# Performance work log

Hardware: AMD Instinct MI355X
Metric: run time of the kernel (lower is better)

## Reference

```python
import jax, jax.numpy as jnp
import numpy as np

E, H, L = 512, 1024, 4
VS, VT = 32000, 32000
B, SS, TT = 64, 48, 48
PAD = 0


def _cell(x, h, c, Wih, Whh, bih, bhh):
    # torch.nn.LSTMCell math: gate order i, f, g, o
    g = x @ Wih.T + h @ Whh.T + bih + bhh
    i, f, gg, o = jnp.split(g, 4, axis=-1)
    c = jax.nn.sigmoid(f) * c + jax.nn.sigmoid(i) * jnp.tanh(gg)
    h = jax.nn.sigmoid(o) * jnp.tanh(c)
    return h, c


def setup_inputs() -> dict:
    key = jax.random.key(0)
    ks = jax.random.split(key, 14)
    s = 0.05
    d = {}
    d['src_tokens'] = jax.random.randint(ks[0], (SS, B), 0, VS, dtype=jnp.int32)
    d['tgt_tokens'] = jax.random.randint(ks[1], (TT, B), 0, VT, dtype=jnp.int32)
    d['src_emb'] = jax.random.normal(ks[2], (VS, E)) * s
    d['tgt_emb'] = jax.random.normal(ks[3], (VT, E)) * s
    d['enc_Wih0'] = jax.random.normal(ks[4], (4 * H, E)) * s
    d['enc_WihR'] = jax.random.normal(ks[5], (L - 1, 4 * H, H)) * s
    d['enc_Whh'] = jax.random.normal(ks[6], (L, 4 * H, H)) * s
    d['enc_bih'] = jnp.zeros((L, 4 * H))
    d['enc_bhh'] = jnp.zeros((L, 4 * H))
    d['dec_Wih0'] = jax.random.normal(ks[7], (4 * H, E + H)) * s
    d['dec_WihR'] = jax.random.normal(ks[8], (L - 1, 4 * H, H)) * s
    d['dec_Whh'] = jax.random.normal(ks[9], (L, 4 * H, H)) * s
    d['dec_bih'] = jnp.zeros((L, 4 * H))
    d['dec_bhh'] = jnp.zeros((L, 4 * H))
    d['att_vec_W'] = jax.random.normal(ks[10], (H, 2 * H)) * s
    d['readout_W'] = jax.random.normal(ks[11], (VT, H)) * s
    return d


def _forward(src_tokens, tgt_tokens, src_emb, tgt_emb, enc_Wih0, enc_WihR,
             enc_Whh, enc_bih, enc_bhh, dec_Wih0, dec_WihR, dec_Whh, dec_bih,
             dec_bhh, att_vec_W, readout_W):
    src_x = src_emb[src_tokens]                      # [SS, B, E]
    h0 = jnp.zeros((L, B, H), src_emb.dtype)
    c0 = jnp.zeros((L, B, H), src_emb.dtype)

    def enc_step(carry, x_t):
        h, c = carry
        inp = x_t
        hs, cs = [], []
        for l in range(L):
            Wih = enc_Wih0 if l == 0 else enc_WihR[l - 1]
            hn, cn = _cell(inp, h[l], c[l], Wih, enc_Whh[l], enc_bih[l], enc_bhh[l])
            hs.append(hn); cs.append(cn)
            inp = hn
        return (jnp.stack(hs), jnp.stack(cs)), inp

    (hT, cT), enc_out = jax.lax.scan(enc_step, (h0, c0), src_x)
    src_enc = enc_out.transpose(1, 0, 2)             # [B, SS, H]

    # decoder init: last encoder layer (h, c) copied to every decoder layer
    hd = jnp.tile(hT[-1][None], (L, 1, 1))
    cd = jnp.tile(cT[-1][None], (L, 1, 1))
    tgt_x = tgt_emb[tgt_tokens[:-1]]                 # [TT-1, B, E]
    att0 = jnp.zeros((B, H), src_emb.dtype)

    def dec_step(carry, y_t):
        h, c, att = carry
        inp = jnp.concatenate([y_t, att], axis=-1)   # input feeding
        hs, cs = [], []
        for l in range(L):
            Wih = dec_Wih0 if l == 0 else dec_WihR[l - 1]
            hn, cn = _cell(inp, h[l], c[l], Wih, dec_Whh[l], dec_bih[l], dec_bhh[l])
            hs.append(hn); cs.append(cn)
            inp = hn
        h_top = hs[-1]
        # global attention, 'dot' score (full-length seqs -> all-zero mask is a no-op)
        scores = jnp.einsum('bsh,bh->bs', src_enc, h_top)
        alpha = jax.nn.softmax(scores, axis=-1)
        ctx = jnp.einsum('bs,bsh->bh', alpha, src_enc)
        att_t = jnp.tanh(jnp.concatenate([h_top, ctx], axis=-1) @ att_vec_W.T)
        return (jnp.stack(hs), jnp.stack(cs), att_t), att_t

    _, att_ves = jax.lax.scan(dec_step, (hd, cd, att0), tgt_x)  # [TT-1, B, H]

    logp = jax.nn.log_softmax(att_ves @ readout_W.T, axis=-1)   # [TT-1, B, VT]
    gold = tgt_tokens[1:]
    gold_lp = jnp.take_along_axis(logp, gold[..., None], axis=-1)[..., 0]
    mask = (gold != PAD).astype(logp.dtype)
    return (gold_lp * mask).sum(axis=0)              # [B]


def reference(src_tokens, tgt_tokens, src_emb, tgt_emb, enc_Wih0, enc_WihR,
              enc_Whh, enc_bih, enc_bhh, dec_Wih0, dec_WihR, dec_Whh, dec_bih,
              dec_bhh, att_vec_W, readout_W):
    return _forward(src_tokens, tgt_tokens, src_emb, tgt_emb, enc_Wih0,
                    enc_WihR, enc_Whh, enc_bih, enc_bhh, dec_Wih0, dec_WihR,
                    dec_Whh, dec_bih, dec_bhh, att_vec_W, readout_W)
```

## Files before the change

kernel.cpp:

```cpp
#include <hip/hip_runtime.h>


typedef __attribute__((ext_vector_type(8))) short bf16x8;
typedef __attribute__((ext_vector_type(4))) float f32x4;

#define SMEM_BYTES 32768
#define SMEM_RO    49152

#define NMT_SYNC_LIGHT()                                   \
  do {                                                     \
    asm volatile("s_waitcnt lgkmcnt(0)" ::: "memory");     \
    __builtin_amdgcn_s_barrier();                          \
    __builtin_amdgcn_sched_barrier(0);                     \
  } while (0)

__device__ __forceinline__ float bf2f(ushort u) {
  union { uint i; float f; } v; v.i = ((uint)u) << 16; return v.f;
}
__device__ __forceinline__ ushort f2bf(float x) {
  union { float f; uint i; } v; v.f = x;
  uint r = (v.i + 0x7fffu + ((v.i >> 16) & 1u)) >> 16;
  return (ushort)r;
}
__device__ __forceinline__ float sigm(float x) {
  return __fdividef(1.f, 1.f + __expf(-x));
}
__device__ __forceinline__ float tanhf_fast(float x) {
  const float e = __expf(2.f * x);
  return 1.f - __fdividef(2.f, e + 1.f);
}

__device__ __forceinline__ void gemm_term(
    const ushort* __restrict__ A, int lda,
    const ushort* __restrict__ W, int ldw,
    int K, int m0, int n0,
    f32x4 acc[4], char* s)
{
  char* sA0 = s;
  char* sB0 = s + 8192;
  char* sA1 = s + 16384;
  char* sB1 = s + 24576;
  const int tid = threadIdx.x;
  const int lane = tid & 63;
  const int w = tid >> 6;
  const int r0 = tid >> 3;
  const int cge = (tid & 7) << 3;
  const ushort* Arow0 = A + (size_t)(m0 + r0) * lda + cge;
  const ushort* Arow1 = A + (size_t)(m0 + r0 + 32) * lda + cge;
  const ushort* Wrow0 = W + (size_t)(n0 + r0) * ldw + cge;
  const ushort* Wrow1 = W + (size_t)(n0 + r0 + 32) * ldw + cge;
  const int so0 = r0 * 128 + (((tid & 7) << 4) ^ ((r0 & 7) << 4));
  const int so1 = so0 + 4096;

  uint4 a0 = *reinterpret_cast<const uint4*>(Arow0);
  uint4 a1 = *reinterpret_cast<const uint4*>(Arow1);
  uint4 b0 = *reinterpret_cast<const uint4*>(Wrow0);
  uint4 b1 = *reinterpret_cast<const uint4*>(Wrow1);
  *reinterpret_cast<uint4*>(sA0 + so0) = a0;
  *reinterpret_cast<uint4*>(sA0 + so1) = a1;
  *reinterpret_cast<uint4*>(sB0 + so0) = b0;
  *reinterpret_cast<uint4*>(sB0 + so1) = b1;
  if (K > 64) {
    a0 = *reinterpret_cast<const uint4*>(Arow0 + 64);
    a1 = *reinterpret_cast<const uint4*>(Arow1 + 64);
    b0 = *reinterpret_cast<const uint4*>(Wrow0 + 64);
    b1 = *reinterpret_cast<const uint4*>(Wrow1 + 64);
  }
  const int axor = (lane & 7) << 4;
  const int arow = (w * 16 + (lane & 15)) * 128;
  const int brow = (lane & 15) * 128;
  const int kb0 = (lane >> 4) << 4;
  for (int kt = 0; kt < K; kt += 64) {
    char* cA = (kt & 64) ? sA1 : sA0;
    char* cB = (kt & 64) ? sB1 : sB0;
    char* nA = (kt & 64) ? sA0 : sA1;
    char* nB = (kt & 64) ? sB0 : sB1;
    __syncthreads();
    if (kt + 64 < K) {
      *reinterpret_cast<uint4*>(nA + so0) = a0;
      *reinterpret_cast<uint4*>(nA + so1) = a1;
      *reinterpret_cast<uint4*>(nB + so0) = b0;
      *reinterpret_cast<uint4*>(nB + so1) = b1;
      if (kt + 128 < K) {
        a0 = *reinterpret_cast<const uint4*>(Arow0 + kt + 128);
        a1 = *reinterpret_cast<const uint4*>(Arow1 + kt + 128);
        b0 = *reinterpret_cast<const uint4*>(Wrow0 + kt + 128);
        b1 = *reinterpret_cast<const uint4*>(Wrow1 + kt + 128);
      }
    }
#pragma unroll
    for (int ks = 0; ks < 2; ++ks) {
      const int kb = ks * 64 + kb0;
      bf16x8 af = *reinterpret_cast<const bf16x8*>(cA + arow + (kb ^ axor));
#pragma unroll
      for (int nf = 0; nf < 4; ++nf) {
        bf16x8 bfr = *reinterpret_cast<const bf16x8*>(
            cB + nf * 2048 + brow + (kb ^ axor));
        acc[nf] = __builtin_amdgcn_mfma_f32_16x16x32_bf16(af, bfr, acc[nf], 0, 0, 0);
      }
    }
  }
  __syncthreads();
}

__device__ __forceinline__ void store_f32(
    float* __restrict__ out, int ldo, int m0, int n0, f32x4 acc[4])
{
  const int tid = threadIdx.x, lane = tid & 63, w = tid >> 6;
  const int rbase = w * 16 + ((lane >> 4) << 2);
  const int cb = lane & 15;
#pragma unroll
  for (int nf = 0; nf < 4; ++nf)
#pragma unroll
    for (int r = 0; r < 4; ++r)
      out[(size_t)(m0 + rbase + r) * ldo + n0 + nf * 16 + cb] = acc[nf][r];
}

__device__ __forceinline__ void cell_store(
    float* smemF, f32x4 acc[4],
    float* __restrict__ c, ushort* __restrict__ hout,
    ushort* __restrict__ senc_t, int j0)
{
  const int tid = threadIdx.x, lane = tid & 63, w = tid >> 6;
  const int rbase = w * 16 + ((lane >> 4) << 2);
  const int cb = lane & 15;
  __syncthreads();
#pragma unroll
  for (int nf = 0; nf < 4; ++nf)
#pragma unroll
    for (int r = 0; r < 4; ++r)
      smemF[(rbase + r) * 68 + nf * 16 + cb] = acc[nf][r];
  __syncthreads();
#pragma unroll
  for (int i = 0; i < 4; ++i) {
    const int id = tid + i * 256;
    const int b = id >> 4, u = id & 15;
    const float g0 = smemF[b * 68 + u * 4 + 0];
    const float g1 = smemF[b * 68 + u * 4 + 1];
    const float g2 = smemF[b * 68 + u * 4 + 2];
    const float g3 = smemF[b * 68 + u * 4 + 3];
    const int off = b * 1024 + j0 + u;
    const float cold = c[off];
    const float cn = sigm(g1) * cold + sigm(g0) * tanhf_fast(g2);
    const float hv = sigm(g3) * tanhf_fast(cn);
    c[off] = cn;
    const ushort hb = f2bf(hv);
    hout[off] = hb;
    if (senc_t) senc_t[(size_t)b * 49152 + j0 + u] = hb;
  }
}

__global__ __launch_bounds__(256) void nmt_init(float* c, ushort* henc, ushort* attbf)
{
  const int idx = blockIdx.x * 256 + threadIdx.x;
  if (idx < 262144) c[idx] = 0.f;
  if (idx < 65536) {
    attbf[idx] = 0;
    henc[idx] = 0;
    henc[(size_t)1 * 49 * 65536 + idx] = 0;
    henc[(size_t)2 * 49 * 65536 + idx] = 0;
    henc[(size_t)3 * 49 * 65536 + idx] = 0;
  }
}

__global__ __launch_bounds__(256) void nmt_convperm(
    const float* __restrict__ in, ushort* __restrict__ out,
    int L, int Kin, int col0, int Kout)
{
  const size_t idx = (size_t)blockIdx.x * 256 + threadIdx.x;
  const size_t total = (size_t)L * 4096 * Kout;
  if (idx >= total) return;
  const int k = (int)(idx % Kout);
  const size_t rem = idx / Kout;
  const int rp = (int)(rem % 4096);
  const int l = (int)(rem / 4096);
  const int j = rp >> 2, g = rp & 3;
  out[idx] = f2bf(in[((size_t)l * 4096 + g * 1024 + j) * Kin + col0 + k]);
}

__global__ __launch_bounds__(256) void nmt_convplain(
    const float* __restrict__ in, ushort* __restrict__ out, size_t n)
{
  const size_t idx = (size_t)blockIdx.x * 256 + threadIdx.x;
  if (idx < n) out[idx] = f2bf(in[idx]);
}

__global__ __launch_bounds__(256) void nmt_bias(
    const float* __restrict__ bih, const float* __restrict__ bhh, float* __restrict__ bc)
{
  const int idx = blockIdx.x * 256 + threadIdx.x;
  if (idx >= 4 * 4096) return;
  const int rp = idx & 4095, l = idx >> 12;
  const int j = rp >> 2, g = rp & 3;
  bc[idx] = bih[l * 4096 + g * 1024 + j] + bhh[l * 4096 + g * 1024 + j];
}

__global__ __launch_bounds__(256) void nmt_gather(
    const int* __restrict__ tok, const float* __restrict__ emb,
    ushort* __restrict__ out, int rows)
{
  const size_t idx = (size_t)blockIdx.x * 256 + threadIdx.x;
  if (idx >= (size_t)rows * 512) return;
  const int k = (int)(idx & 511);
  const int r = (int)(idx >> 9);
  out[idx] = f2bf(emb[(size_t)tok[r] * 512 + k]);
}

__global__ __launch_bounds__(256) void nmt_pre(
    const ushort* __restrict__ A, const ushort* __restrict__ Wp,
    const float* __restrict__ bc0, float* __restrict__ out, int K)
{
  __shared__ __align__(16) char smem[SMEM_BYTES];
  const int m0 = blockIdx.x * 64, n0 = blockIdx.y * 64;
  const int lane = threadIdx.x & 63;
  const int cb = lane & 15;
  f32x4 acc[4];
#pragma unroll
  for (int nf = 0; nf < 4; ++nf) {
    const float bv = bc0[n0 + nf * 16 + cb];
#pragma unroll
    for (int r = 0; r < 4; ++r) acc[nf][r] = bv;
  }
  gemm_term(A, K, Wp, K, K, m0, n0, acc, smem);
  store_f32(out, 4096, m0, n0, acc);
}

__global__ __launch_bounds__(256) void nmt_decinit(
    const ushort* __restrict__ henc, float* c, ushort* h)
{
  const int idx = blockIdx.x * 256 + threadIdx.x;
  if (idx >= 65536) return;
  const ushort hv = henc[((size_t)3 * 49 + 48) * 65536 + idx];
  const float cv = c[3 * 65536 + idx];
  c[idx] = cv; c[65536 + idx] = cv; c[2 * 65536 + idx] = cv;
  h[idx] = hv; h[65536 + idx] = hv; h[2 * 65536 + idx] = hv; h[3 * 65536 + idx] = hv;
}

__global__ __launch_bounds__(256) void nmt_sv(
    const ushort* __restrict__ senc, const ushort* __restrict__ attW,
    ushort* __restrict__ SV)
{
  __shared__ __align__(16) char smem[SMEM_BYTES];
  const int b = blockIdx.x;
  const int n0 = blockIdx.y * 64;
  const int tid = threadIdx.x, lane = tid & 63, w = tid >> 6;
  const int rbase = w * 16 + ((lane >> 4) << 2), cb = lane & 15;
  f32x4 acc[4];
#pragma unroll
  for (int nf = 0; nf < 4; ++nf)
#pragma unroll
    for (int r = 0; r < 4; ++r) acc[nf][r] = 0.f;
  gemm_term(senc + (size_t)b * 49152, 1024, attW + 1024, 2048, 1024, 0, n0,
            acc, smem);
#pragma unroll
  for (int nf = 0; nf < 4; ++nf)
#pragma unroll
    for (int r = 0; r < 4; ++r) {
      const int row = rbase + r;
      if (row < 48)
        SV[(size_t)b * 49152 + row * 1024 + n0 + nf * 16 + cb] = f2bf(acc[nf][r]);
    }
}

__global__ __launch_bounds__(256) void nmt_enc_tick(
    int v, int lc0, int ncell, int lp0,
    ushort* __restrict__ henc, ushort* __restrict__ srcenc,
    float* __restrict__ c,
    const ushort* __restrict__ WihR, const ushort* __restrict__ Whh,
    const float* __restrict__ X0, const float* __restrict__ bcE,
    float* __restrict__ pbufE)
{
  __shared__ __align__(16) char smem[SMEM_BYTES];
  const int n0 = blockIdx.x * 64;
  const int tid = threadIdx.x, lane = tid & 63, w = tid >> 6;
  const int rbase = w * 16 + ((lane >> 4) << 2), cb = lane & 15;
  f32x4 acc[4];
  if ((int)blockIdx.y < ncell) {
    const int l = lc0 + blockIdx.y;
    const int t = v - 2 * l;
    if (l == 0) {
#pragma unroll
      for (int nf = 0; nf < 4; ++nf)
#pragma unroll
        for (int r = 0; r < 4; ++r)
          acc[nf][r] = X0[(size_t)t * 262144 + (size_t)(rbase + r) * 4096 + n0 + nf * 16 + cb];
    } else {
#pragma unroll
      for (int nf = 0; nf < 4; ++nf)
#pragma unroll
        for (int r = 0; r < 4; ++r)
          acc[nf][r] = pbufE[(size_t)l * 262144 + (size_t)(rbase + r) * 4096 + n0 + nf * 16 + cb];
    }
    gemm_term(henc + ((size_t)l * 49 + t) * 65536, 1024,
              Whh + (size_t)l * 4194304, 1024, 1024, 0, n0, acc, smem);
    cell_store((float*)smem, acc, c + l * 65536,
               henc + ((size_t)l * 49 + t + 1) * 65536,
               (l == 3) ? (srcenc + t * 1024) : (ushort*)nullptr, n0 >> 2);
  } else {
    const int l = lp0 + (blockIdx.y - ncell);
    const int tp = v + 1 - 2 * l;
#pragma unroll
    for (int nf = 0; nf < 4; ++nf) {
      const float bv = bcE[l * 4096 + n0 + nf * 16 + cb];
#pragma unroll
      for (int r = 0; r < 4; ++r) acc[nf][r] = bv;
    }
    gemm_term(henc + ((size_t)(l - 1) * 49 + tp + 1) * 65536, 1024,
              WihR + (size_t)(l - 1) * 4194304, 1024, 1024, 0, n0, acc, smem);
    store_f32(pbufE + (size_t)l * 262144, 4096, 0, n0, acc);
  }
}

__global__ __launch_bounds__(256) void nmt_dec_stage(
    int l, const ushort* __restrict__ hp, ushort* __restrict__ hn,
    float* __restrict__ c,
    const ushort* __restrict__ Whh, const ushort* __restrict__ WihR,
    const ushort* __restrict__ Wd0a, const ushort* __restrict__ attbf,
    const float* __restrict__ Y0t, const float* __restrict__ bcD,
    float* __restrict__ pbuf)
{
  __shared__ __align__(16) char smem[SMEM_BYTES];
  const int n0 = blockIdx.x * 64;
  const int tid = threadIdx.x, lane = tid & 63, w = tid >> 6;
  const int rbase = w * 16 + ((lane >> 4) << 2), cb = lane & 15;
  f32x4 acc[4];
  if (blockIdx.y == 0) {
    if (l == 0) {
#pragma unroll
      for (int nf = 0; nf < 4; ++nf)
#pragma unroll
        for (int r = 0; r < 4; ++r) {
          const size_t o = (size_t)(rbase + r) * 4096 + n0 + nf * 16 + cb;
          acc[nf][r] = Y0t[o] + pbuf[o];
        }
      gemm_term(attbf, 1024, Wd0a, 1024, 1024, 0, n0, acc, smem);
    } else {
#pragma unroll
      for (int nf = 0; nf < 4; ++nf)
#pragma unroll
        for (int r = 0; r < 4; ++r)
          acc[nf][r] = pbuf[(size_t)l * 262144 + (size_t)(rbase + r) * 4096 + n0 + nf * 16 + cb];
      gemm_term(hn + (l - 1) * 65536, 1024, WihR + (size_t)(l - 1) * 4194304,
                1024, 1024, 0, n0, acc, smem);
    }
    cell_store((float*)smem, acc, c + l * 65536, hn + l * 65536,
               (ushort*)nullptr, n0 >> 2);
  } else {
    const int lp = (l + 1) & 3;
    if (lp == 0) {
#pragma unroll
      for (int nf = 0; nf < 4; ++nf)
#pragma unroll
        for (int r = 0; r < 4; ++r) acc[nf][r] = 0.f;
      gemm_term(hn, 1024, Whh, 1024, 1024, 0, n0, acc, smem);
    } else {
#pragma unroll
      for (int nf = 0; nf < 4; ++nf) {
        const float bv = bcD[lp * 4096 + n0 + nf * 16 + cb];
#pragma unroll
        for (int r = 0; r < 4; ++r) acc[nf][r] = bv;
      }
      gemm_term(hp + lp * 65536, 1024, Whh + (size_t)lp * 4194304,
                1024, 1024, 0, n0, acc, smem);
    }
    store_f32(pbuf + (size_t)lp * 262144, 4096, 0, n0, acc);
  }
}

__global__ __launch_bounds__(256) void nmt_partial0(
    const ushort* __restrict__ h0, const ushort* __restrict__ Whh0,
    float* __restrict__ pbuf)
{
  __shared__ __align__(16) char smem[SMEM_BYTES];
  const int n0 = blockIdx.x * 64;
  f32x4 acc[4];
#pragma unroll
  for (int nf = 0; nf < 4; ++nf)
#pragma unroll
    for (int r = 0; r < 4; ++r) acc[nf][r] = 0.f;
  gemm_term(h0, 1024, Whh0, 1024, 1024, 0, n0, acc, smem);
  store_f32(pbuf, 4096, 0, n0, acc);
}

__global__ __launch_bounds__(256) void nmt_attnAB(
    const ushort* __restrict__ h3, const ushort* __restrict__ senc,
    const ushort* __restrict__ SV, const ushort* __restrict__ attW,
    float* __restrict__ ctx2, float* __restrict__ hb)
{
  __shared__ __align__(16) char smem[SMEM_BYTES];
  const int bid = blockIdx.x;
  const int tid = threadIdx.x, lane = tid & 63, w = tid >> 6;
  if (bid < 64) {
    float* sc = (float*)smem;
    float* al = (float*)smem + 64;
    const int b = bid;
    const ushort* sb = senc + (size_t)b * 49152;
    const ushort* vb = SV + (size_t)b * 49152;
    float hreg[16];
#pragma unroll
    for (int q = 0; q < 16; ++q) hreg[q] = bf2f(h3[b * 1024 + lane * 16 + q]);
    for (int s = w; s < 48; s += 4) {
      const ushort* vr = sb + s * 1024 + lane * 16;
      float p = 0.f;
#pragma unroll
      for (int q = 0; q < 16; ++q) p += bf2f(vr[q]) * hreg[q];
      for (int d = 1; d < 64; d <<= 1) p += __shfl_xor(p, d);
      if (lane == 0) sc[s] = p;
    }
    __syncthreads();
    if (tid < 64) {
      const float v = (lane < 48) ? sc[lane] : -3.4e38f;
      float m = v;
      for (int d = 1; d < 64; d <<= 1) m = fmaxf(m, __shfl_xor(m, d));
      float e = (lane < 48) ? expf(v - m) : 0.f;
      float s = e;
      for (int d = 1; d < 64; d <<= 1) s += __shfl_xor(s, d);
      al[lane] = e / s;
    }
    __syncthreads();
    const int k0 = tid * 4;
    float a0 = 0, a1 = 0, a2 = 0, a3 = 0;
    for (int s = 0; s < 48; ++s) {
      const float als = al[s];
      const ushort* vr = vb + s * 1024 + k0;
      a0 += als * bf2f(vr[0]); a1 += als * bf2f(vr[1]);
      a2 += als * bf2f(vr[2]); a3 += als * bf2f(vr[3]);
    }
    ctx2[b * 1024 + k0 + 0] = a0; ctx2[b * 1024 + k0 + 1] = a1;
    ctx2[b * 1024 + k0 + 2] = a2; ctx2[b * 1024 + k0 + 3] = a3;
  } else {
    const int n0 = (bid - 64) * 64;
    f32x4 acc[4];
#pragma unroll
    for (int nf = 0; nf < 4; ++nf)
#pragma unroll
      for (int r = 0; r < 4; ++r) acc[nf][r] = 0.f;
    gemm_term(h3, 1024, attW, 2048, 1024, 0, n0, acc, smem);
    store_f32(hb, 1024, 0, n0, acc);
  }
}

__global__ __launch_bounds__(256) void nmt_attnSB(
    const float* __restrict__ ctx2, const float* __restrict__ hb,
    ushort* __restrict__ attbf, ushort* __restrict__ av_t)
{
  const int base = blockIdx.x * 1024 + threadIdx.x * 4;
#pragma unroll
  for (int k = 0; k < 4; ++k) {
    const int i = base + k;
    const ushort us = f2bf(tanhf_fast(hb[i] + ctx2[i]));
    attbf[i] = us;
    av_t[i] = us;
  }
}

__global__ __launch_bounds__(256) void nmt_readout(
    const ushort* __restrict__ attves, const ushort* __restrict__ routW,
    const int* __restrict__ tgt, float* __restrict__ pmax,
    float* __restrict__ psum, float* __restrict__ goldl)
{
  __shared__ __align__(16) char smem[SMEM_RO];
  const int g = blockIdx.x;
  const int n0 = blockIdx.y * 64;
  const int tid = threadIdx.x, lane = tid & 63, w = tid >> 6;
  const int rbase = w * 16 + ((lane >> 4) << 2), cb = lane & 15;
  const int r0 = tid >> 3;
  const int cge = (tid & 7) << 3;
  const int soX = r0 * 128 + (((tid & 7) << 4) ^ ((r0 & 7) << 4));
  const int axor = (lane & 7) << 4;
  const int arow = (w * 16 + (lane & 15)) * 128;
  const int brow = (lane & 15) * 128;
  const int kb0 = (lane >> 4) << 4;

  const ushort* A0r0 = attves + (size_t)(g * 128 + r0) * 1024 + cge;
  const ushort* A0r1 = attves + (size_t)(g * 128 + r0 + 32) * 1024 + cge;
  const ushort* A1r0 = attves + (size_t)(g * 128 + 64 + r0) * 1024 + cge;
  const ushort* A1r1 = attves + (size_t)(g * 128 + 64 + r0 + 32) * 1024 + cge;
  const ushort* Br0  = routW + (size_t)(n0 + r0) * 1024 + cge;
  const ushort* Br1  = routW + (size_t)(n0 + r0 + 32) * 1024 + cge;

  f32x4 acc[2][4];
#pragma unroll
  for (int mi = 0; mi < 2; ++mi)
#pragma unroll
    for (int nf = 0; nf < 4; ++nf)
#pragma unroll
      for (int r = 0; r < 4; ++r) acc[mi][nf][r] = 0.f;

  uint4 ra0 = *(const uint4*)(A0r0);
  uint4 ra1 = *(const uint4*)(A0r1);
  uint4 ra2 = *(const uint4*)(A1r0);
  uint4 ra3 = *(const uint4*)(A1r1);
  uint4 rb0 = *(const uint4*)(Br0);
  uint4 rb1 = *(const uint4*)(Br1);
  {
    char* sl = smem;
    *(uint4*)(sl + soX) = ra0;          *(uint4*)(sl + 4096 + soX) = ra1;
    *(uint4*)(sl + 8192 + soX) = ra2;   *(uint4*)(sl + 12288 + soX) = ra3;
    *(uint4*)(sl + 16384 + soX) = rb0;  *(uint4*)(sl + 20480 + soX) = rb1;
  }
  ra0 = *(const uint4*)(A0r0 + 64);
  ra1 = *(const uint4*)(A0r1 + 64);
  ra2 = *(const uint4*)(A1r0 + 64);
  ra3 = *(const uint4*)(A1r1 + 64);
  rb0 = *(const uint4*)(Br0 + 64);
  rb1 = *(const uint4*)(Br1 + 64);

  for (int kt = 0; kt < 1024; kt += 64) {
    NMT_SYNC_LIGHT();
    if (kt + 64 < 1024) {
      char* sl = smem + ((((kt >> 6) + 1) & 1) ? 24576 : 0);
      *(uint4*)(sl + soX) = ra0;          *(uint4*)(sl + 4096 + soX) = ra1;
      *(uint4*)(sl + 8192 + soX) = ra2;   *(uint4*)(sl + 12288 + soX) = ra3;
      *(uint4*)(sl + 16384 + soX) = rb0;  *(uint4*)(sl + 20480 + soX) = rb1;
      if (kt + 128 < 1024) {
        ra0 = *(const uint4*)(A0r0 + kt + 128);
        ra1 = *(const uint4*)(A0r1 + kt + 128);
        ra2 = *(const uint4*)(A1r0 + kt + 128);
        ra3 = *(const uint4*)(A1r1 + kt + 128);
        rb0 = *(const uint4*)(Br0 + kt + 128);
        rb1 = *(const uint4*)(Br1 + kt + 128);
      }
    }
    char* cur = smem + (((kt >> 6) & 1) ? 24576 : 0);
#pragma unroll
    for (int ks = 0; ks < 2; ++ks) {
      const int kb = (ks << 6) + kb0;
      bf16x8 bf0 = *(const bf16x8*)(cur + 16384 + 0 * 2048 + brow + (kb ^ axor));
      bf16x8 bf1 = *(const bf16x8*)(cur + 16384 + 1 * 2048 + brow + (kb ^ axor));
      bf16x8 bf2 = *(const bf16x8*)(cur + 16384 + 2 * 2048 + brow + (kb ^ axor));
      bf16x8 bf3 = *(const bf16x8*)(cur + 16384 + 3 * 2048 + brow + (kb ^ axor));
      bf16x8 af0 = *(const bf16x8*)(cur + arow + (kb ^ axor));
      bf16x8 af1 = *(const bf16x8*)(cur + 8192 + arow + (kb ^ axor));
      acc[0][0] = __builtin_amdgcn_mfma_f32_16x16x32_bf16(af0, bf0, acc[0][0], 0, 0, 0);
      acc[0][1] = __builtin_amdgcn_mfma_f32_16x16x32_bf16(af0, bf1, acc[0][1], 0, 0, 0);
      acc[0][2] = __builtin_amdgcn_mfma_f32_16x16x32_bf16(af0, bf2, acc[0][2], 0, 0, 0);
      acc[0][3] = __builtin_amdgcn_mfma_f32_16x16x32_bf16(af0, bf3, acc[0][3], 0, 0, 0);
      acc[1][0] = __builtin_amdgcn_mfma_f32_16x16x32_bf16(af1, bf0, acc[1][0], 0, 0, 0);
      acc[1][1] = __builtin_amdgcn_mfma_f32_16x16x32_bf16(af1, bf1, acc[1][1], 0, 0, 0);
      acc[1][2] = __builtin_amdgcn_mfma_f32_16x16x32_bf16(af1, bf2, acc[1][2], 0, 0, 0);
      acc[1][3] = __builtin_amdgcn_mfma_f32_16x16x32_bf16(af1, bf3, acc[1][3], 0, 0, 0);
    }
  }

#pragma unroll
  for (int mi = 0; mi < 2; ++mi) {
    const int gm = g * 2 + mi;
    if (gm >= 47) continue;
#pragma unroll
    for (int r = 0; r < 4; ++r) {
      float lm = fmaxf(fmaxf(acc[mi][0][r], acc[mi][1][r]),
                       fmaxf(acc[mi][2][r], acc[mi][3][r]));
      for (int d = 1; d < 16; d <<= 1) lm = fmaxf(lm, __shfl_xor(lm, d));
      float ls = 0.f;
#pragma unroll
      for (int nf = 0; nf < 4; ++nf) ls += expf(acc[mi][nf][r] - lm);
      for (int d = 1; d < 16; d <<= 1) ls += __shfl_xor(ls, d);
      const int grow = gm * 64 + rbase + r;
      if (cb == 0) {
        pmax[(size_t)grow * 500 + blockIdx.y] = lm;
        psum[(size_t)grow * 500 + blockIdx.y] = ls;
      }
      const int t = grow >> 6, b = grow & 63;
      const int gold = tgt[(t + 1) * 64 + b];
#pragma unroll
      for (int nf = 0; nf < 4; ++nf)
        if (n0 + nf * 16 + cb == gold) goldl[grow] = acc[mi][nf][r];
    }
  }
}

__global__ __launch_bounds__(64) void nmt_combine(
    const float* __restrict__ pmax, const float* __restrict__ psum,
    const float* __restrict__ goldl, const int* __restrict__ tgt,
    float* __restrict__ lpm)
{
  const int row = blockIdx.x;
  const int lane = threadIdx.x;
  float m = -3.4e38f, s = 0.f;
  for (int i = lane; i < 500; i += 64) {
    const float pm = pmax[(size_t)row * 500 + i];
    const float ps = psum[(size_t)row * 500 + i];
    if (pm > m) { s = s * expf(m - pm) + ps; m = pm; }
    else        { s += ps * expf(pm - m); }
  }
  for (int d = 1; d < 64; d <<= 1) {
    const float om = __shfl_xor(m, d), os = __shfl_xor(s, d);
    if (om > m) { s = s * expf(m - om) + os; m = om; }
    else        { s += os * expf(om - m); }
  }
  if (lane == 0) {
    const int t = row >> 6, b = row & 63;
    const int gold = tgt[(t + 1) * 64 + b];
    const float lp = goldl[row] - m - logf(s);
    lpm[row] = (gold != 0) ? lp : 0.f;
  }
}

__global__ __launch_bounds__(64) void nmt_final(
    const float* __restrict__ lpm, float* __restrict__ out)
{
  const int b = threadIdx.x;
  float s = 0.f;
  for (int t = 0; t < 47; ++t) s += lpm[t * 64 + b];
  out[b] = s;
}

extern "C" void kernel_launch(void* const* d_in, const int* in_sizes, int n_in,
                              void* d_out, int out_size, void* d_ws, size_t ws_size,
                              hipStream_t stream)
{
  (void)in_sizes; (void)n_in; (void)out_size; (void)ws_size;
  const int*   src_tok  = (const int*)d_in[0];
  const int*   tgt_tok  = (const int*)d_in[1];
  const float* src_emb  = (const float*)d_in[2];
  const float* tgt_emb  = (const float*)d_in[3];
  const float* eWih0    = (const float*)d_in[4];
  const float* eWihR    = (const float*)d_in[5];
  const float* eWhh     = (const float*)d_in[6];
  const float* ebih     = (const float*)d_in[7];
  const float* ebhh     = (const float*)d_in[8];
  const float* dWih0    = (const float*)d_in[9];
  const float* dWihR    = (const float*)d_in[10];
  const float* dWhh     = (const float*)d_in[11];
  const float* dbih     = (const float*)d_in[12];
  const float* dbhh     = (const float*)d_in[13];
  const float* attW_f   = (const float*)d_in[14];
  const float* routW_f  = (const float*)d_in[15];

  char* p = (char*)d_ws;
  auto alloc = [&](size_t bytes) { void* r = (void*)p; p += (bytes + 255) & ~(size_t)255; return r; };
  ushort* eWih0p = (ushort*)alloc((size_t)4096 * 512 * 2);
  ushort* eWihRp = (ushort*)alloc((size_t)3 * 4096 * 1024 * 2);
  ushort* eWhhp  = (ushort*)alloc((size_t)4 * 4096 * 1024 * 2);
  ushort* dWih0y = (ushort*)alloc((size_t)4096 * 512 * 2);
  ushort* dWih0a = (ushort*)alloc((size_t)4096 * 1024 * 2);
  ushort* dWihRp = (ushort*)alloc((size_t)3 * 4096 * 1024 * 2);
  ushort* dWhhp  = (ushort*)alloc((size_t)4 * 4096 * 1024 * 2);
  ushort* attWb  = (ushort*)alloc((size_t)1024 * 2048 * 2);
  ushort* routWb = (ushort*)alloc((size_t)32000 * 1024 * 2);
  ushort* srcx   = (ushort*)alloc((size_t)3072 * 512 * 2);
  ushort* tgtx   = (ushort*)alloc((size_t)3008 * 512 * 2);
  ushort* henc   = (ushort*)alloc((size_t)4 * 49 * 65536 * 2);
  ushort* hA     = (ushort*)alloc((size_t)4 * 65536 * 2);
  ushort* hB     = (ushort*)alloc((size_t)4 * 65536 * 2);
  ushort* srcenc = (ushort*)alloc((size_t)64 * 49152 * 2);
  ushort* SVbuf  = (ushort*)alloc((size_t)64 * 49152 * 2);
  ushort* attbf  = (ushort*)alloc((size_t)65536 * 2);
  ushort* attves = (ushort*)alloc((size_t)3072 * 1024 * 2);
  float*  ctx2   = (float*)alloc((size_t)65536 * 4);
  float*  hbuf   = (float*)alloc((size_t)65536 * 4);
  float*  pbuf   = (float*)alloc((size_t)4 * 262144 * 4);
  float*  pbufE  = (float*)alloc((size_t)4 * 262144 * 4);
  float*  X0     = (float*)alloc((size_t)3072 * 4096 * 4);
  float*  Y0     = (float*)alloc((size_t)3008 * 4096 * 4);
  float*  bcE    = (float*)alloc((size_t)16384 * 4);
  float*  bcD    = (float*)alloc((size_t)16384 * 4);
  float*  cbuf   = (float*)alloc((size_t)4 * 65536 * 4);
  float*  pmaxb  = (float*)alloc((size_t)3008 * 500 * 4);
  float*  psumb  = (float*)alloc((size_t)3008 * 500 * 4);
  float*  goldl  = (float*)alloc((size_t)3008 * 4);
  float*  lpm    = (float*)alloc((size_t)3008 * 4);

  const dim3 B256(256);
  auto g1 = [](size_t n) { return dim3((unsigned)((n + 255) / 256)); };

  nmt_init<<<g1(262144), B256, 0, stream>>>(cbuf, henc, attbf);

  nmt_convperm<<<g1((size_t)4096 * 512), B256, 0, stream>>>(eWih0, eWih0p, 1, 512, 0, 512);
  nmt_convperm<<<g1((size_t)3 * 4096 * 1024), B256, 0, stream>>>(eWihR, eWihRp, 3, 1024, 0, 1024);
  nmt_convperm<<<g1((size_t)4 * 4096 * 1024), B256, 0, stream>>>(eWhh, eWhhp, 4, 1024, 0, 1024);
  nmt_convperm<<<g1((size_t)4096 * 512), B256, 0, stream>>>(dWih0, dWih0y, 1, 1536, 0, 512);
  nmt_convperm<<<g1((size_t)4096 * 1024), B256, 0, stream>>>(dWih0, dWih0a, 1, 1536, 512, 1024);
  nmt_convperm<<<g1((size_t)3 * 4096 * 1024), B256, 0, stream>>>(dWihR, dWihRp, 3, 1024, 0, 1024);
  nmt_convperm<<<g1((size_t)4 * 4096 * 1024), B256, 0, stream>>>(dWhh, dWhhp, 4, 1024, 0, 1024);
  nmt_convplain<<<g1((size_t)1024 * 2048), B256, 0, stream>>>(attW_f, attWb, (size_t)1024 * 2048);
  nmt_convplain<<<g1((size_t)32000 * 1024), B256, 0, stream>>>(routW_f, routWb, (size_t)32000 * 1024);
  nmt_bias<<<g1(16384), B256, 0, stream>>>(ebih, ebhh, bcE);
  nmt_bias<<<g1(16384), B256, 0, stream>>>(dbih, dbhh, bcD);
  nmt_gather<<<g1((size_t)3072 * 512), B256, 0, stream>>>(src_tok, src_emb, srcx, 3072);
  nmt_gather<<<g1((size_t)3008 * 512), B256, 0, stream>>>(tgt_tok, tgt_emb, tgtx, 3008);

  nmt_pre<<<dim3(48, 64), B256, 0, stream>>>(srcx, eWih0p, bcE, X0, 512);
  nmt_pre<<<dim3(47, 64), B256, 0, stream>>>(tgtx, dWih0y, bcD, Y0, 512);

  for (int v = 0; v < 54; ++v) {
    int lc0 = (v > 47) ? ((v - 47 + 1) / 2) : 0;
    int lc1 = (v / 2 < 3) ? (v / 2) : 3;
    int ncell = lc1 - lc0 + 1;
    int lp0 = (v + 1 > 47) ? ((v + 1 - 47 + 1) / 2) : 1;
    if (lp0 < 1) lp0 = 1;
    int lp1 = ((v + 1) / 2 < 3) ? ((v + 1) / 2) : 3;
    int npart = (lp1 >= lp0) ? (lp1 - lp0 + 1) : 0;
    nmt_enc_tick<<<dim3(64, ncell + npart), B256, 0, stream>>>(
        v, lc0, ncell, lp0, henc, srcenc, cbuf, eWihRp, eWhhp, X0, bcE, pbufE);
  }
  nmt_decinit<<<g1(65536), B256, 0, stream>>>(henc, cbuf, hA);
  nmt_sv<<<dim3(64, 16), B256, 0, stream>>>(srcenc, attWb, SVbuf);
  nmt_partial0<<<dim3(64), B256, 0, stream>>>(hA, dWhhp, pbuf);

  for (int t = 0; t < 47; ++t) {
    ushort* hp = (t & 1) ? hB : hA;
    ushort* hn = (t & 1) ? hA : hB;
    for (int l = 0; l < 4; ++l) {
      nmt_dec_stage<<<dim3(64, 2), B256, 0, stream>>>(
          l, hp, hn, cbuf, dWhhp, dWihRp, dWih0a, attbf,
          Y0 + (size_t)t * 262144, bcD, pbuf);
    }
    nmt_attnAB<<<dim3(80), B256, 0, stream>>>(hn + 3 * 65536, srcenc, SVbuf,
                                              attWb, ctx2, hbuf);
    nmt_attnSB<<<dim3(64), B256, 0, stream>>>(ctx2, hbuf, attbf,
                                              attves + (size_t)t * 65536);
  }

  nmt_readout<<<dim3(24, 500), B256, 0, stream>>>(attves, routWb, tgt_tok,
                                                  pmaxb, psumb, goldl);
  nmt_combine<<<dim3(3008), dim3(64), 0, stream>>>(pmaxb, psumb, goldl, tgt_tok, lpm);
  nmt_final<<<dim3(1), dim3(64), 0, stream>>>(lpm, (float*)d_out);
}
```

Before: 3.993 ms.

## Enlarge readout M tile to 192 rows and merge decoder prep kernels

The readout GEMM now processes three 64-row fragments per block instead of two. This cuts the number of row groups and the repeated reads of the readout weight tile, at the cost of 64KB of shared memory and more accumulator registers, which may lower occupancy. The decoder-init, source-projection and first-partial kernels are combined into one launch to cut launch overhead, with the partial GEMM reading the encoder's last hidden state directly.

New measurement: 3.997 ms. About the same (+0.1%).

```diff
diff --git a/kernel.cpp b/kernel.cpp
--- a/kernel.cpp
+++ b/kernel.cpp
@@ -5,7 +5,7 @@
 typedef __attribute__((ext_vector_type(4))) float f32x4;
 
 #define SMEM_BYTES 32768
-#define SMEM_RO    49152
+#define SMEM_RO    65536
 
 #define NMT_SYNC_LIGHT()                                   \
   do {                                                     \
@@ -225,41 +225,51 @@
   store_f32(out, 4096, m0, n0, acc);
 }
 
-__global__ __launch_bounds__(256) void nmt_decinit(
-    const ushort* __restrict__ henc, float* c, ushort* h)
-{
-  const int idx = blockIdx.x * 256 + threadIdx.x;
-  if (idx >= 65536) return;
-  const ushort hv = henc[((size_t)3 * 49 + 48) * 65536 + idx];
-  const float cv = c[3 * 65536 + idx];
-  c[idx] = cv; c[65536 + idx] = cv; c[2 * 65536 + idx] = cv;
-  h[idx] = hv; h[65536 + idx] = hv; h[2 * 65536 + idx] = hv; h[3 * 65536 + idx] = hv;
-}
-
-__global__ __launch_bounds__(256) void nmt_sv(
-    const ushort* __restrict__ senc, const ushort* __restrict__ attW,
-    ushort* __restrict__ SV)
+__global__ __launch_bounds__(256) void nmt_prep2(
+    const ushort* __restrict__ henc, const ushort* __restrict__ srcenc,
+    const ushort* __restrict__ attW, const ushort* __restrict__ Whh0,
+    ushort* __restrict__ SV, float* __restrict__ c, ushort* __restrict__ h,
+    float* __restrict__ pbuf)
 {
   __shared__ __align__(16) char smem[SMEM_BYTES];
-  const int b = blockIdx.x;
-  const int n0 = blockIdx.y * 64;
+  const int bid = blockIdx.x;
   const int tid = threadIdx.x, lane = tid & 63, w = tid >> 6;
   const int rbase = w * 16 + ((lane >> 4) << 2), cb = lane & 15;
-  f32x4 acc[4];
-#pragma unroll
-  for (int nf = 0; nf < 4; ++nf)
-#pragma unroll
-    for (int r = 0; r < 4; ++r) acc[nf][r] = 0.f;
-  gemm_term(senc + (size_t)b * 49152, 1024, attW + 1024, 2048, 1024, 0, n0,
-            acc, smem);
-#pragma unroll
-  for (int nf = 0; nf < 4; ++nf)
-#pragma unroll
-    for (int r = 0; r < 4; ++r) {
-      const int row = rbase + r;
-      if (row < 48)
-        SV[(size_t)b * 49152 + row * 1024 + n0 + nf * 16 + cb] = f2bf(acc[nf][r]);
-    }
+  if (bid < 1024) {
+    const int b = bid >> 4;
+    const int n0 = (bid & 15) * 64;
+    f32x4 acc[4];
+#pragma unroll
+    for (int nf = 0; nf < 4; ++nf)
+#pragma unroll
+      for (int r = 0; r < 4; ++r) acc[nf][r] = 0.f;
+    gemm_term(srcenc + (size_t)b * 49152, 1024, attW + 1024, 2048, 1024, 0, n0,
+              acc, smem);
+#pragma unroll
+    for (int nf = 0; nf < 4; ++nf)
+#pragma unroll
+      for (int r = 0; r < 4; ++r) {
+        const int row = rbase + r;
+        if (row < 48)
+          SV[(size_t)b * 49152 + row * 1024 + n0 + nf * 16 + cb] = f2bf(acc[nf][r]);
+      }
+  } else if (bid < 1280) {
+    const int idx = (bid - 1024) * 256 + tid;
+    const ushort hv = henc[((size_t)3 * 49 + 48) * 65536 + idx];
+    const float cv = c[3 * 65536 + idx];
+    c[idx] = cv; c[65536 + idx] = cv; c[2 * 65536 + idx] = cv;
+    h[idx] = hv; h[65536 + idx] = hv; h[2 * 65536 + idx] = hv; h[3 * 65536 + idx] = hv;
+  } else {
+    const int n0 = (bid - 1280) * 64;
+    f32x4 acc[4];
+#pragma unroll
+    for (int nf = 0; nf < 4; ++nf)
+#pragma unroll
+      for (int r = 0; r < 4; ++r) acc[nf][r] = 0.f;
+    gemm_term(henc + ((size_t)3 * 49 + 48) * 65536, 1024, Whh0, 1024, 1024,
+              0, n0, acc, smem);
+    store_f32(pbuf, 4096, 0, n0, acc);
+  }
 }
 
 __global__ __launch_bounds__(256) void nmt_enc_tick(
@@ -365,21 +375,6 @@
     }
     store_f32(pbuf + (size_t)lp * 262144, 4096, 0, n0, acc);
   }
-}
-
-__global__ __launch_bounds__(256) void nmt_partial0(
-    const ushort* __restrict__ h0, const ushort* __restrict__ Whh0,
-    float* __restrict__ pbuf)
-{
-  __shared__ __align__(16) char smem[SMEM_BYTES];
-  const int n0 = blockIdx.x * 64;
-  f32x4 acc[4];
-#pragma unroll
-  for (int nf = 0; nf < 4; ++nf)
-#pragma unroll
-    for (int r = 0; r < 4; ++r) acc[nf][r] = 0.f;
-  gemm_term(h0, 1024, Whh0, 1024, 1024, 0, n0, acc, smem);
-  store_f32(pbuf, 4096, 0, n0, acc);
 }
 
 __global__ __launch_bounds__(256) void nmt_attnAB(
@@ -472,16 +467,18 @@
   const int brow = (lane & 15) * 128;
   const int kb0 = (lane >> 4) << 4;
 
-  const ushort* A0r0 = attves + (size_t)(g * 128 + r0) * 1024 + cge;
-  const ushort* A0r1 = attves + (size_t)(g * 128 + r0 + 32) * 1024 + cge;
-  const ushort* A1r0 = attves + (size_t)(g * 128 + 64 + r0) * 1024 + cge;
-  const ushort* A1r1 = attves + (size_t)(g * 128 + 64 + r0 + 32) * 1024 + cge;
+  const ushort* A0r0 = attves + (size_t)(g * 192 + r0) * 1024 + cge;
+  const ushort* A0r1 = attves + (size_t)(g * 192 + r0 + 32) * 1024 + cge;
+  const ushort* A1r0 = attves + (size_t)(g * 192 + 64 + r0) * 1024 + cge;
+  const ushort* A1r1 = attves + (size_t)(g * 192 + 64 + r0 + 32) * 1024 + cge;
+  const ushort* A2r0 = attves + (size_t)(g * 192 + 128 + r0) * 1024 + cge;
+  const ushort* A2r1 = attves + (size_t)(g * 192 + 128 + r0 + 32) * 1024 + cge;
   const ushort* Br0  = routW + (size_t)(n0 + r0) * 1024 + cge;
   const ushort* Br1  = routW + (size_t)(n0 + r0 + 32) * 1024 + cge;
 
-  f32x4 acc[2][4];
-#pragma unroll
-  for (int mi = 0; mi < 2; ++mi)
+  f32x4 acc[3][4];
+#pragma unroll
+  for (int mi = 0; mi < 3; ++mi)
 #pragma unroll
     for (int nf = 0; nf < 4; ++nf)
 #pragma unroll
@@ -491,47 +488,56 @@
   uint4 ra1 = *(const uint4*)(A0r1);
   uint4 ra2 = *(const uint4*)(A1r0);
   uint4 ra3 = *(const uint4*)(A1r1);
+  uint4 ra4 = *(const uint4*)(A2r0);
+  uint4 ra5 = *(const uint4*)(A2r1);
   uint4 rb0 = *(const uint4*)(Br0);
   uint4 rb1 = *(const uint4*)(Br1);
   {
     char* sl = smem;
     *(uint4*)(sl + soX) = ra0;          *(uint4*)(sl + 4096 + soX) = ra1;
     *(uint4*)(sl + 8192 + soX) = ra2;   *(uint4*)(sl + 12288 + soX) = ra3;
-    *(uint4*)(sl + 16384 + soX) = rb0;  *(uint4*)(sl + 20480 + soX) = rb1;
+    *(uint4*)(sl + 16384 + soX) = ra4;  *(uint4*)(sl + 20480 + soX) = ra5;
+    *(uint4*)(sl + 24576 + soX) = rb0;  *(uint4*)(sl + 28672 + soX) = rb1;
   }
   ra0 = *(const uint4*)(A0r0 + 64);
   ra1 = *(const uint4*)(A0r1 + 64);
   ra2 = *(const uint4*)(A1r0 + 64);
   ra3 = *(const uint4*)(A1r1 + 64);
+  ra4 = *(const uint4*)(A2r0 + 64);
+  ra5 = *(const uint4*)(A2r1 + 64);
   rb0 = *(const uint4*)(Br0 + 64);
   rb1 = *(const uint4*)(Br1 + 64);
 
   for (int kt = 0; kt < 1024; kt += 64) {
     NMT_SYNC_LIGHT();
     if (kt + 64 < 1024) {
-      char* sl = smem + ((((kt >> 6) + 1) & 1) ? 24576 : 0);
+      char* sl = smem + ((((kt >> 6) + 1) & 1) ? 32768 : 0);
       *(uint4*)(sl + soX) = ra0;          *(uint4*)(sl + 4096 + soX) = ra1;
       *(uint4*)(sl + 8192 + soX) = ra2;   *(uint4*)(sl + 12288 + soX) = ra3;
-      *(uint4*)(sl + 16384 + soX) = rb0;  *(uint4*)(sl + 20480 + soX) = rb1;
+      *(uint4*)(sl + 16384 + soX) = ra4;  *(uint4*)(sl + 20480 + soX) = ra5;
+      *(uint4*)(sl + 24576 + soX) = rb0;  *(uint4*)(sl + 28672 + soX) = rb1;
       if (kt + 128 < 1024) {
         ra0 = *(const uint4*)(A0r0 + kt + 128);
         ra1 = *(const uint4*)(A0r1 + kt + 128);
         ra2 = *(const uint4*)(A1r0 + kt + 128);
         ra3 = *(const uint4*)(A1r1 + kt + 128);
+        ra4 = *(const uint4*)(A2r0 + kt + 128);
+        ra5 = *(const uint4*)(A2r1 + kt + 128);
         rb0 = *(const uint4*)(Br0 + kt + 128);
         rb1 = *(const uint4*)(Br1 + kt + 128);
       }
     }
-    char* cur = smem + (((kt >> 6) & 1) ? 24576 : 0);
+    char* cur = smem + (((kt >> 6) & 1) ? 32768 : 0);
 #pragma unroll
     for (int ks = 0; ks < 2; ++ks) {
       const int kb = (ks << 6) + kb0;
-      bf16x8 bf0 = *(const bf16x8*)(cur + 16384 + 0 * 2048 + brow + (kb ^ axor));
-      bf16x8 bf1 = *(const bf16x8*)(cur + 16384 + 1 * 2048 + brow + (kb ^ axor));
-      bf16x8 bf2 = *(const bf16x8*)(cur + 16384 + 2 * 2048 + brow + (kb ^ axor));
-      bf16x8 bf3 = *(const bf16x8*)(cur + 16384 + 3 * 2048 + brow + (kb ^ axor));
+      bf16x8 bf0 = *(const bf16x8*)(cur + 24576 + 0 * 2048 + brow + (kb ^ axor));
+      bf16x8 bf1 = *(const bf16x8*)(cur + 24576 + 1 * 2048 + brow + (kb ^ axor));
+      bf16x8 bf2 = *(const bf16x8*)(cur + 24576 + 2 * 2048 + brow + (kb ^ axor));
+      bf16x8 bf3 = *(const bf16x8*)(cur + 24576 + 3 * 2048 + brow + (kb ^ axor));
       bf16x8 af0 = *(const bf16x8*)(cur + arow + (kb ^ axor));
       bf16x8 af1 = *(const bf16x8*)(cur + 8192 + arow + (kb ^ axor));
+      bf16x8 af2 = *(const bf16x8*)(cur + 16384 + arow + (kb ^ axor));
       acc[0][0] = __builtin_amdgcn_mfma_f32_16x16x32_bf16(af0, bf0, acc[0][0], 0, 0, 0);
       acc[0][1] = __builtin_amdgcn_mfma_f32_16x16x32_bf16(af0, bf1, acc[0][1], 0, 0, 0);
       acc[0][2] = __builtin_amdgcn_mfma_f32_16x16x32_bf16(af0, bf2, acc[0][2], 0, 0, 0);
@@ -540,12 +546,16 @@
       acc[1][1] = __builtin_amdgcn_mfma_f32_16x16x32_bf16(af1, bf1, acc[1][1], 0, 0, 0);
       acc[1][2] = __builtin_amdgcn_mfma_f32_16x16x32_bf16(af1, bf2, acc[1][2], 0, 0, 0);
       acc[1][3] = __builtin_amdgcn_mfma_f32_16x16x32_bf16(af1, bf3, acc[1][3], 0, 0, 0);
-    }
-  }
-
-#pragma unroll
-  for (int mi = 0; mi < 2; ++mi) {
-    const int gm = g * 2 + mi;
+      acc[2][0] = __builtin_amdgcn_mfma_f32_16x16x32_bf16(af2, bf0, acc[2][0], 0, 0, 0);
+      acc[2][1] = __builtin_amdgcn_mfma_f32_16x16x32_bf16(af2, bf1, acc[2][1], 0, 0, 0);
+      acc[2][2] = __builtin_amdgcn_mfma_f32_16x16x32_bf16(af2, bf2, acc[2][2], 0, 0, 0);
+      acc[2][3] = __builtin_amdgcn_mfma_f32_16x16x32_bf16(af2, bf3, acc[2][3], 0, 0, 0);
+    }
+  }
+
+#pragma unroll
+  for (int mi = 0; mi < 3; ++mi) {
+    const int gm = g * 3 + mi;
     if (gm >= 47) continue;
 #pragma unroll
     for (int r = 0; r < 4; ++r) {
@@ -695,9 +705,8 @@
     nmt_enc_tick<<<dim3(64, ncell + npart), B256, 0, stream>>>(
         v, lc0, ncell, lp0, henc, srcenc, cbuf, eWihRp, eWhhp, X0, bcE, pbufE);
   }
-  nmt_decinit<<<g1(65536), B256, 0, stream>>>(henc, cbuf, hA);
-  nmt_sv<<<dim3(64, 16), B256, 0, stream>>>(srcenc, attWb, SVbuf);
-  nmt_partial0<<<dim3(64), B256, 0, stream>>>(hA, dWhhp, pbuf);
+  nmt_prep2<<<dim3(1344), B256, 0, stream>>>(henc, srcenc, attWb, dWhhp,
+                                             SVbuf, cbuf, hA, pbuf);
 
   for (int t = 0; t < 47; ++t) {
     ushort* hp = (t & 1) ? hB : hA;
@@ -713,7 +722,7 @@
                                               attves + (size_t)t * 65536);
   }
 
-  nmt_readout<<<dim3(24, 500), B256, 0, stream>>>(attves, routWb, tgt_tok,
+  nmt_readout<<<dim3(16, 500), B256, 0, stream>>>(attves, routWb, tgt_tok,
                                                   pmaxb, psumb, goldl);
   nmt_combine<<<dim3(3008), dim3(64), 0, stream>>>(pmaxb, psumb, goldl, tgt_tok, lpm);
   nmt_final<<<dim3(1), dim3(64), 0, stream>>>(lpm, (float*)d_out);
```
